# Optimization experiments

Measured on AMD Instinct MI355X. Metric: run time of the kernel, lower is better.

Reference implementation:

```python
import jax, jax.numpy as jnp
import numpy as np

N = 50000      # num_nodes
E = 300000     # edges per edge type
T = 3          # num_edge_type
C = 2          # num_channels
F_IN = 64      # feature_size
HID = 64       # hidden_size (w_out)
NL = 2         # num_layers (GT layers per FastGTN)
BETA = 0.5     # gtn_beta
TP = 0.8       # teleport_probability


def setup_inputs() -> dict:
    key = jax.random.key(0)
    ks = jax.random.split(key, 16)
    X = jax.random.normal(ks[0], (N, F_IN), dtype=jnp.float32)
    edge_index_0 = jax.random.randint(ks[1], (2, E), 0, N)
    edge_index_1 = jax.random.randint(ks[2], (2, E), 0, N)
    edge_index_2 = jax.random.randint(ks[3], (2, E), 0, N)
    edge_value_0 = jax.random.uniform(ks[4], (E,), dtype=jnp.float32)
    edge_value_1 = jax.random.uniform(ks[5], (E,), dtype=jnp.float32)
    edge_value_2 = jax.random.uniform(ks[6], (E,), dtype=jnp.float32)
    # glorot for Ws (per-channel projection), std=0.1 for GT layer mixing weights
    g0 = np.sqrt(6.0 / (F_IN + HID))
    g1 = np.sqrt(6.0 / (HID + HID))
    Ws0 = jax.random.uniform(ks[7], (C, F_IN, HID), minval=-g0, maxval=g0, dtype=jnp.float32)
    Ws1 = jax.random.uniform(ks[8], (C, HID, HID), minval=-g1, maxval=g1, dtype=jnp.float32)
    layerW0 = 0.1 * jax.random.normal(ks[9], (NL, C, T), dtype=jnp.float32)
    layerW1 = 0.1 * jax.random.normal(ks[10], (NL, C, T), dtype=jnp.float32)
    gl = np.sqrt(1.0 / (C * HID))
    lin_W0 = jax.random.uniform(ks[11], (C * HID, HID), minval=-gl, maxval=gl, dtype=jnp.float32)
    lin_b0 = jax.random.uniform(ks[12], (HID,), minval=-gl, maxval=gl, dtype=jnp.float32)
    lin_W1 = jax.random.uniform(ks[13], (C * HID, HID), minval=-gl, maxval=gl, dtype=jnp.float32)
    lin_b1 = jax.random.uniform(ks[14], (HID,), minval=-gl, maxval=gl, dtype=jnp.float32)
    return dict(X=X,
                edge_value_0=edge_value_0, edge_value_1=edge_value_1, edge_value_2=edge_value_2,
                Ws0=Ws0, Ws1=Ws1, layerW0=layerW0, layerW1=layerW1,
                lin_W0=lin_W0, lin_b0=lin_b0, lin_W1=lin_W1, lin_b1=lin_b1,
                edge_index_0=edge_index_0, edge_index_1=edge_index_1, edge_index_2=edge_index_2)


def _spmm_mix(H, filt, vals, etype, row, col):
    # H: [C, N, d]; filt: [C, T] softmaxed; vals: [Etot]; etype/row/col: [Etot]
    # == for each channel c: sum_j filt[c,j] * (A_j @ H[c])
    w = vals[None, :] * filt[:, etype]          # [C, Etot]
    msg = w[:, :, None] * H[:, col, :]          # [C, Etot, d]
    return jax.vmap(lambda m: jax.ops.segment_sum(m, row, num_segments=N))(msg)


def _fastgtn_block(Xin, Ws, layerW, linW, linb, row, col, vals, etype):
    H = jnp.einsum('nf,cfo->cno', Xin, Ws)      # [C, N, HID]
    X0 = jax.lax.stop_gradient(H)               # X_ = H.clone().detach()
    for l in range(NL):
        filt = jax.nn.softmax(layerW[l], axis=1)
        H = _spmm_mix(H, filt, vals, etype, row, col)
    Hm = TP * jax.nn.relu(BETA * X0 + (1.0 - BETA) * H) + (1.0 - TP) * X0
    Hm = jnp.transpose(Hm, (1, 0, 2)).reshape(N, C * Hm.shape[-1])  # [N, C*HID]
    return jax.nn.relu(Hm @ linW + linb)


def reference(X, edge_value_0, edge_value_1, edge_value_2,
              Ws0, Ws1, layerW0, layerW1,
              lin_W0, lin_b0, lin_W1, lin_b1,
              edge_index_0, edge_index_1, edge_index_2):
    row = jnp.concatenate([edge_index_0[0], edge_index_1[0], edge_index_2[0]])
    col = jnp.concatenate([edge_index_0[1], edge_index_1[1], edge_index_2[1]])
    vals = jnp.concatenate([edge_value_0, edge_value_1, edge_value_2])
    etype = jnp.repeat(jnp.arange(T), E)
    H = _fastgtn_block(X, Ws0, layerW0, lin_W0, lin_b0, row, col, vals, etype)
    H = _fastgtn_block(H, Ws1, layerW1, lin_W1, lin_b1, row, col, vals, etype)
    return H
```

## Files before the change

### kernel.cpp

```cpp
#include <hip/hip_runtime.h>
#include <hip/hip_fp16.h>

#define NN 50000
#define EE 300000
#define ETOT (3 * EE)
#define HD 64
#define RB 256
#define NB 196
#define CHUNK 8192
#define NBLKT ((EE + CHUNK - 1) / CHUNK)
#define NBT (3 * NBLKT)
#define NTOT (NB * NBT)
#define GS_VPT ((NTOT + 1023) / 1024)
#define MAXB 6144
#define PROJ_NTILE (NN / 16)
#define PP_GRID (NBT + 512)


__global__ void __launch_bounds__(256)
hist1_kernel(const int* __restrict__ ei0, const int* __restrict__ ei1,
             const int* __restrict__ ei2, int* __restrict__ hist) {
    __shared__ int lh[NB];
    int t = blockIdx.y;
    const int* ei = (t == 0) ? ei0 : (t == 1) ? ei1 : ei2;
    int tid = threadIdx.x;
    for (int i = tid; i < NB; i += 256) lh[i] = 0;
    __syncthreads();
    int e0 = blockIdx.x * CHUNK;
    for (int it = 0; it < CHUNK / 256; ++it) {
        int e = e0 + it * 256 + tid;
        if (e < EE) atomicAdd(&lh[ei[e] >> 8], 1);
    }
    __syncthreads();
    int flat = t * NBLKT + blockIdx.x;
    for (int i = tid; i < NB; i += 256) hist[i * NBT + flat] = lh[i];
}

__global__ void __launch_bounds__(1024)
gscan_kernel(const int* __restrict__ hist, int* __restrict__ gbase,
             int* __restrict__ bbase, int* __restrict__ rp,
             const float* __restrict__ lw0, const float* __restrict__ lw1,
             float* __restrict__ filt) {
    __shared__ int wsum[16];
    int tid = threadIdx.x, lane = tid & 63, wv = tid >> 6;
    if (tid < 8) {
        int b = tid >> 2, l = (tid >> 1) & 1, c = tid & 1;
        const float* lw = (b == 0 ? lw0 : lw1) + l * 6 + c * 3;
        float a0 = lw[0], a1 = lw[1], a2 = lw[2];
        float m  = fmaxf(a0, fmaxf(a1, a2));
        float e0 = expf(a0 - m), e1 = expf(a1 - m), e2 = expf(a2 - m);
        float s  = e0 + e1 + e2;
        float* o = filt + tid * 3;
        o[0] = e0 / s; o[1] = e1 / s; o[2] = e2 / s;
    }
    int s0 = tid * GS_VPT;
    int local = 0;
    for (int j = 0; j < GS_VPT; ++j) {
        int s = s0 + j;
        if (s < NTOT) local += hist[s];
    }
    int x = local;
#pragma unroll
    for (int d = 1; d < 64; d <<= 1) {
        int y = __shfl_up(x, d);
        if (lane >= d) x += y;
    }
    if (lane == 63) wsum[wv] = x;
    __syncthreads();
    if (tid == 0) {
        int s = 0;
        for (int i = 0; i < 16; ++i) { int t = wsum[i]; wsum[i] = s; s += t; }
    }
    __syncthreads();
    int run = x + wsum[wv] - local;
    for (int j = 0; j < GS_VPT; ++j) {
        int s = s0 + j;
        if (s < NTOT) {
            gbase[s] = run;
            int bucket = s / NBT;
            if (s - bucket * NBT == 0) bbase[bucket] = run;
            run += hist[s];
        }
    }
    if (tid == 0) { bbase[NB] = ETOT; rp[NN] = ETOT; }
}

__global__ void __launch_bounds__(256)
place_proj_kernel(const int* __restrict__ ei0, const int* __restrict__ ei1,
                  const int* __restrict__ ei2,
                  const float* __restrict__ ev0, const float* __restrict__ ev1,
                  const float* __restrict__ ev2,
                  const int* __restrict__ gbase, uint2* __restrict__ staged,
                  const float* __restrict__ Xin, const float* __restrict__ Ws,
                  __half2* __restrict__ Hh) {
    __shared__ float Wl[2 * 64 * 64];
    __shared__ float Xs[16 * 65];
    __shared__ int   lbase[NB];
    int tid = threadIdx.x;

    if (blockIdx.x < NBT) {
        int flat = blockIdx.x;
        int t  = flat / NBLKT;
        int bx = flat - t * NBLKT;
        const int*   ei = (t == 0) ? ei0 : (t == 1) ? ei1 : ei2;
        const float* ev = (t == 0) ? ev0 : (t == 1) ? ev1 : ev2;
        for (int i = tid; i < NB; i += 256) lbase[i] = gbase[i * NBT + flat];
        __syncthreads();
        int e0 = bx * CHUNK;
        for (int it = 0; it < CHUNK / 256; ++it) {
            int e = e0 + it * 256 + tid;
            if (e < EE) {
                int row = ei[e];
                int col = ei[EE + e];
                unsigned int q = (unsigned int)__float2int_rn(ev[e] * 16383.0f);
                unsigned int mw = (unsigned int)col | ((unsigned int)t << 16) | (q << 18);
                int pos = atomicAdd(&lbase[row >> 8], 1);
                staged[pos] = make_uint2(mw, (unsigned int)row);
            }
        }
    } else {
        for (int i = tid; i < 2 * 64 * 64; i += 256) Wl[i] = Ws[i];
        int oq = (tid & 15) * 4;
        int ln = tid >> 4;
        for (int tile = blockIdx.x - NBT; tile < PROJ_NTILE; tile += 512) {
            int n0 = tile * 16;
            __syncthreads();
            for (int i = tid; i < 16 * 64; i += 256)
                Xs[(i >> 6) * 65 + (i & 63)] = Xin[(n0 + (i >> 6)) * 64 + (i & 63)];
            __syncthreads();
            float a0[4] = {0.f, 0.f, 0.f, 0.f};
            float a1[4] = {0.f, 0.f, 0.f, 0.f};
            for (int f = 0; f < 64; ++f) {
                float  x  = Xs[ln * 65 + f];
                float4 w0 = *(const float4*)&Wl[f * 64 + oq];
                float4 w1 = *(const float4*)&Wl[4096 + f * 64 + oq];
                a0[0] += x * w0.x; a0[1] += x * w0.y;
                a0[2] += x * w0.z; a0[3] += x * w0.w;
                a1[0] += x * w1.x; a1[1] += x * w1.y;
                a1[2] += x * w1.z; a1[3] += x * w1.w;
            }
            float4 o4;
            ((__half2*)&o4)[0] = __floats2half2_rn(a0[0], a1[0]);
            ((__half2*)&o4)[1] = __floats2half2_rn(a0[1], a1[1]);
            ((__half2*)&o4)[2] = __floats2half2_rn(a0[2], a1[2]);
            ((__half2*)&o4)[3] = __floats2half2_rn(a0[3], a1[3]);
            *(float4*)&Hh[(n0 + ln) * HD + oq] = o4;
        }
    }
}

__global__ void __launch_bounds__(256)
csr_kernel(const uint2* __restrict__ staged, const int* __restrict__ bbase,
           int* __restrict__ rp, unsigned int* __restrict__ meta) {
    __shared__ int hist[RB];
    __shared__ int lcur[RB];
    __shared__ int wsum[4];
    __shared__ unsigned int metaL[MAXB];
    int b   = blockIdx.x;
    int tid = threadIdx.x;
    int base = bbase[b];
    int cnt  = bbase[b + 1] - base;
    int row0 = b * RB;

    hist[tid] = 0;
    __syncthreads();
    for (int i = tid; i < cnt; i += 256) {
        uint2 s = staged[base + i];
        atomicAdd(&hist[(int)s.y - row0], 1);
    }
    __syncthreads();
    int lane = tid & 63, wv = tid >> 6;
    int v = hist[tid];
    int x = v;
#pragma unroll
    for (int d = 1; d < 64; d <<= 1) {
        int y = __shfl_up(x, d);
        if (lane >= d) x += y;
    }
    if (lane == 63) wsum[wv] = x;
    __syncthreads();
    if (tid == 0) {
        int s = 0;
        for (int i = 0; i < 4; ++i) { int t = wsum[i]; wsum[i] = s; s += t; }
    }
    __syncthreads();
    int excl = x + wsum[wv] - v;
    lcur[tid] = excl;
    int row = row0 + tid;
    if (row < NN) rp[row] = base + excl;
    __syncthreads();
    for (int i = tid; i < cnt; i += 256) {
        uint2 s = staged[base + i];
        int p = atomicAdd(&lcur[(int)s.y - row0], 1);
        metaL[p] = s.x;
    }
    __syncthreads();
    for (int i = tid; i < cnt; i += 256)
        meta[base + i] = metaL[i];
}

__device__ __forceinline__ void edge_acc(unsigned int mm, float4 r,
                                         float F00, float F01, float F02,
                                         float F10, float F11, float F12,
                                         float* accA, float* accB) {
    int   et = (mm >> 16) & 3;
    float q  = (float)(mm >> 18);
    float w0 = q * ((et == 0) ? F00 : (et == 1) ? F01 : F02);
    float w1 = q * ((et == 0) ? F10 : (et == 1) ? F11 : F12);
#pragma unroll
    for (int i = 0; i < 4; ++i) {
        float2 x = __half22float2(((const __half2*)&r)[i]);
        accA[i] += w0 * x.x;
        accB[i] += w1 * x.y;
    }
}

__global__ void __launch_bounds__(256)
spmm_kernel(const float4* __restrict__ Hin4, float4* __restrict__ Hout4,
            const unsigned int* __restrict__ meta, const int* __restrict__ rp,
            const float* __restrict__ filt ) {
    const int wid  = threadIdx.x >> 6;
    const int lane = threadIdx.x & 63;
    const int g    = lane >> 4;
    const int fq   = lane & 15;
    const int row  = blockIdx.x * 4 + wid;

    const float s = 1.0f / 16383.0f;
    const float F00 = filt[0] * s, F01 = filt[1] * s, F02 = filt[2] * s;
    const float F10 = filt[3] * s, F11 = filt[4] * s, F12 = filt[5] * s;

    float accA[4] = {0.f, 0.f, 0.f, 0.f};
    float accB[4] = {0.f, 0.f, 0.f, 0.f};

    const int beg = rp[row], end = rp[row + 1];
    for (int j0 = beg; j0 < end; j0 += 64) {
        int cnt = min(end - j0, 64);
        unsigned int m = (lane < cnt) ? meta[j0 + lane] : 0u;
        for (int k = 0; k < cnt; k += 24) {
            unsigned int mmA = (unsigned int)__shfl((int)m, k + g);
            unsigned int mmB = (unsigned int)__shfl((int)m, k + 4 + g);
            float4 rA = Hin4[(mmA & 0xffffu) * 16 + fq];
            float4 rB = Hin4[(mmB & 0xffffu) * 16 + fq];
            if (k + 16 < cnt) {
                unsigned int mmC = (unsigned int)__shfl((int)m, k + 8 + g);
                unsigned int mmD = (unsigned int)__shfl((int)m, k + 12 + g);
                unsigned int mmE = (unsigned int)__shfl((int)m, k + 16 + g);
                unsigned int mmF = (unsigned int)__shfl((int)m, k + 20 + g);
                float4 rC = Hin4[(mmC & 0xffffu) * 16 + fq];
                float4 rD = Hin4[(mmD & 0xffffu) * 16 + fq];
                float4 rE = Hin4[(mmE & 0xffffu) * 16 + fq];
                float4 rF = Hin4[(mmF & 0xffffu) * 16 + fq];
                edge_acc(mmA, rA, F00, F01, F02, F10, F11, F12, accA, accB);
                edge_acc(mmB, rB, F00, F01, F02, F10, F11, F12, accA, accB);
                edge_acc(mmC, rC, F00, F01, F02, F10, F11, F12, accA, accB);
                edge_acc(mmD, rD, F00, F01, F02, F10, F11, F12, accA, accB);
                edge_acc(mmE, rE, F00, F01, F02, F10, F11, F12, accA, accB);
                edge_acc(mmF, rF, F00, F01, F02, F10, F11, F12, accA, accB);
            } else if (k + 8 < cnt) {
                unsigned int mmC = (unsigned int)__shfl((int)m, k + 8 + g);
                unsigned int mmD = (unsigned int)__shfl((int)m, k + 12 + g);
                float4 rC = Hin4[(mmC & 0xffffu) * 16 + fq];
                float4 rD = Hin4[(mmD & 0xffffu) * 16 + fq];
                edge_acc(mmA, rA, F00, F01, F02, F10, F11, F12, accA, accB);
                edge_acc(mmB, rB, F00, F01, F02, F10, F11, F12, accA, accB);
                edge_acc(mmC, rC, F00, F01, F02, F10, F11, F12, accA, accB);
                edge_acc(mmD, rD, F00, F01, F02, F10, F11, F12, accA, accB);
            } else {
                edge_acc(mmA, rA, F00, F01, F02, F10, F11, F12, accA, accB);
                edge_acc(mmB, rB, F00, F01, F02, F10, F11, F12, accA, accB);
            }
        }
    }
#pragma unroll
    for (int i = 0; i < 4; ++i) {
        accA[i] += __shfl_xor(accA[i], 16); accA[i] += __shfl_xor(accA[i], 32);
        accB[i] += __shfl_xor(accB[i], 16); accB[i] += __shfl_xor(accB[i], 32);
    }
    if (g == 0) {
        float4 o4;
        ((__half2*)&o4)[0] = __floats2half2_rn(accA[0], accB[0]);
        ((__half2*)&o4)[1] = __floats2half2_rn(accA[1], accB[1]);
        ((__half2*)&o4)[2] = __floats2half2_rn(accA[2], accB[2]);
        ((__half2*)&o4)[3] = __floats2half2_rn(accA[3], accB[3]);
        Hout4[row * 16 + fq] = o4;
    }
}

#define EPI_TILE 64
#define HS_STRIDE 133
template<bool PROJ>
__global__ void __launch_bounds__(256, 4)
epilogue_kernel(const __half2* __restrict__ X0, const __half2* __restrict__ H,
                const float* __restrict__ linW, const float* __restrict__ linb,
                const float* __restrict__ Wsn, float* __restrict__ out,
                __half2* __restrict__ X0out) {
    __shared__ float Hs[EPI_TILE * HS_STRIDE];
    int tid = threadIdx.x;
    int oc = (tid & 15) * 4;
    int nq = tid >> 4;
    float bias[4];
#pragma unroll
    for (int i = 0; i < 4; ++i) bias[i] = linb[oc + i];
    const int ntiles = (NN + EPI_TILE - 1) / EPI_TILE;
    for (int tile = blockIdx.x; tile < ntiles; tile += gridDim.x) {
        int n0 = tile * EPI_TILE;
        __syncthreads();
        for (int i = tid; i < EPI_TILE * 64; i += 256) {
            int ln = i >> 6, d = i & 63;
            int n = n0 + ln;
            float2 x0 = make_float2(0.f, 0.f), h = make_float2(0.f, 0.f);
            if (n < NN) {
                x0 = __half22float2(X0[n * HD + d]);
                h  = __half22float2(H [n * HD + d]);
            }
            float z0 = fmaxf(0.5f * x0.x + 0.5f * h.x, 0.f);
            float z1 = fmaxf(0.5f * x0.y + 0.5f * h.y, 0.f);
            Hs[ln * HS_STRIDE + d]      = 0.8f * z0 + 0.2f * x0.x;
            Hs[ln * HS_STRIDE + 64 + d] = 0.8f * z1 + 0.2f * x0.y;
        }
        __syncthreads();
        float acc[4][4];
#pragma unroll
        for (int j = 0; j < 4; ++j)
#pragma unroll
            for (int i = 0; i < 4; ++i) acc[j][i] = bias[i];
        for (int k = 0; k < 128; ++k) {
            float4 w4 = *(const float4*)&linW[k * 64 + oc];
#pragma unroll
            for (int j = 0; j < 4; ++j) {
                float x = Hs[(nq + 16 * j) * HS_STRIDE + k];
                acc[j][0] += x * w4.x; acc[j][1] += x * w4.y;
                acc[j][2] += x * w4.z; acc[j][3] += x * w4.w;
            }
        }
        if (!PROJ) {
#pragma unroll
            for (int j = 0; j < 4; ++j) {
                int n = n0 + nq + 16 * j;
                if (n < NN) {
#pragma unroll
                    for (int i = 0; i < 4; ++i)
                        out[n * HD + oc + i] = fmaxf(acc[j][i], 0.f);
                }
            }
        } else {
            __syncthreads();
#pragma unroll
            for (int j = 0; j < 4; ++j)
#pragma unroll
                for (int i = 0; i < 4; ++i)
                    Hs[(nq + 16 * j) * HS_STRIDE + oc + i] =
                        fmaxf(acc[j][i], 0.f);
            __syncthreads();
            float p0[4][4], p1[4][4];
#pragma unroll
            for (int j = 0; j < 4; ++j)
#pragma unroll
                for (int i = 0; i < 4; ++i) { p0[j][i] = 0.f; p1[j][i] = 0.f; }
            for (int f = 0; f < 64; ++f) {
                float4 w0 = *(const float4*)&Wsn[f * 64 + oc];
                float4 w1 = *(const float4*)&Wsn[4096 + f * 64 + oc];
#pragma unroll
                for (int j = 0; j < 4; ++j) {
                    float x = Hs[(nq + 16 * j) * HS_STRIDE + f];
                    p0[j][0] += x * w0.x; p0[j][1] += x * w0.y;
                    p0[j][2] += x * w0.z; p0[j][3] += x * w0.w;
                    p1[j][0] += x * w1.x; p1[j][1] += x * w1.y;
                    p1[j][2] += x * w1.z; p1[j][3] += x * w1.w;
                }
            }
#pragma unroll
            for (int j = 0; j < 4; ++j) {
                int n = n0 + nq + 16 * j;
                if (n < NN) {
                    float4 o4;
                    ((__half2*)&o4)[0] = __floats2half2_rn(p0[j][0], p1[j][0]);
                    ((__half2*)&o4)[1] = __floats2half2_rn(p0[j][1], p1[j][1]);
                    ((__half2*)&o4)[2] = __floats2half2_rn(p0[j][2], p1[j][2]);
                    ((__half2*)&o4)[3] = __floats2half2_rn(p0[j][3], p1[j][3]);
                    *(float4*)&X0out[n * HD + oc] = o4;
                }
            }
        }
    }
}

extern "C" void kernel_launch(void* const* d_in, const int* in_sizes, int n_in,
                              void* d_out, int out_size, void* d_ws, size_t ws_size,
                              hipStream_t stream) {
    const float* X     = (const float*)d_in[0];
    const float* ev0   = (const float*)d_in[1];
    const float* ev1   = (const float*)d_in[2];
    const float* ev2   = (const float*)d_in[3];
    const float* Ws0   = (const float*)d_in[4];
    const float* Ws1   = (const float*)d_in[5];
    const float* lw0   = (const float*)d_in[6];
    const float* lw1   = (const float*)d_in[7];
    const float* linW0 = (const float*)d_in[8];
    const float* linb0 = (const float*)d_in[9];
    const float* linW1 = (const float*)d_in[10];
    const float* linb1 = (const float*)d_in[11];
    const int*   ei0   = (const int*)d_in[12];
    const int*   ei1   = (const int*)d_in[13];
    const int*   ei2   = (const int*)d_in[14];
    float* out = (float*)d_out;

    float* ws = (float*)d_ws;
    __half2* X0h = (__half2*)(ws);
    __half2* Ha  = (__half2*)(ws + 1 * NN * HD);
    __half2* Hb  = (__half2*)(ws + 2 * NN * HD);
    uint2*   staged = (uint2*)(ws + 3 * NN * HD);
    float*   filt   = ws + 4 * NN * HD;
    int*     hist   = (int*)(filt + 32);
    int*     gbase  = hist + NTOT;
    int*     bbase  = gbase + NTOT;
    int*     rp     = bbase + NB + 4;
    unsigned int* meta = (unsigned int*)(rp + NN + 16);

    dim3 egrid(NBLKT, 3);
    hist1_kernel<<<egrid, 256, 0, stream>>>(ei0, ei1, ei2, hist);
    gscan_kernel<<<1, 1024, 0, stream>>>(hist, gbase, bbase, rp,
                                         lw0, lw1, filt);
    place_proj_kernel<<<PP_GRID, 256, 0, stream>>>(ei0, ei1, ei2,
                                                   ev0, ev1, ev2,
                                                   gbase, staged,
                                                   X, Ws0, X0h);
    csr_kernel<<<NB, 256, 0, stream>>>(staged, bbase, rp, meta);

    spmm_kernel<<<NN / 4, 256, 0, stream>>>((const float4*)X0h, (float4*)Ha,
                                            meta, rp, filt + 0);
    spmm_kernel<<<NN / 4, 256, 0, stream>>>((const float4*)Ha, (float4*)Hb,
                                            meta, rp, filt + 6);
    epilogue_kernel<true><<<784, 256, 0, stream>>>(X0h, Hb, linW0, linb0,
                                                   Ws1, nullptr, X0h);

    spmm_kernel<<<NN / 4, 256, 0, stream>>>((const float4*)X0h, (float4*)Ha,
                                            meta, rp, filt + 12);
    spmm_kernel<<<NN / 4, 256, 0, stream>>>((const float4*)Ha, (float4*)Hb,
                                            meta, rp, filt + 18);
    epilogue_kernel<false><<<784, 256, 0, stream>>>(X0h, Hb, linW1, linb1,
                                                    Ws1, out, nullptr);
}
```

Measured before the change: 356.0 us.

## Move input projection from place kernel into CSR build kernel

Splits the combined edge-placement/projection kernel into a standalone place kernel and merges the projection blocks into the CSR-build kernel instead. The projection now co-runs with the per-bucket CSR sort rather than with edge placement. It also stops staging the Ws weights in shared memory and reads them straight from global memory, cutting shared memory use so more blocks can be resident alongside the large metaL buffer. The risk is more global/cache traffic for weight reads and uneven load, since only 196 CSR blocks share the launch with 512 projection blocks.

```diff
diff --git a/kernel.cpp b/kernel.cpp
--- a/kernel.cpp
+++ b/kernel.cpp
@@ -14,7 +14,7 @@
 #define GS_VPT ((NTOT + 1023) / 1024)
 #define MAXB 6144
 #define PROJ_NTILE (NN / 16)
-#define PP_GRID (NBT + 512)
+#define CP_GRID (NB + 512)
 
 
 __global__ void __launch_bounds__(256)
@@ -86,43 +86,91 @@
 }
 
 __global__ void __launch_bounds__(256)
-place_proj_kernel(const int* __restrict__ ei0, const int* __restrict__ ei1,
-                  const int* __restrict__ ei2,
-                  const float* __restrict__ ev0, const float* __restrict__ ev1,
-                  const float* __restrict__ ev2,
-                  const int* __restrict__ gbase, uint2* __restrict__ staged,
-                  const float* __restrict__ Xin, const float* __restrict__ Ws,
-                  __half2* __restrict__ Hh) {
-    __shared__ float Wl[2 * 64 * 64];
+place_kernel(const int* __restrict__ ei0, const int* __restrict__ ei1,
+             const int* __restrict__ ei2,
+             const float* __restrict__ ev0, const float* __restrict__ ev1,
+             const float* __restrict__ ev2,
+             const int* __restrict__ gbase, uint2* __restrict__ staged) {
+    __shared__ int lbase[NB];
+    int tid = threadIdx.x;
+    int flat = blockIdx.x;
+    int t  = flat / NBLKT;
+    int bx = flat - t * NBLKT;
+    const int*   ei = (t == 0) ? ei0 : (t == 1) ? ei1 : ei2;
+    const float* ev = (t == 0) ? ev0 : (t == 1) ? ev1 : ev2;
+    for (int i = tid; i < NB; i += 256) lbase[i] = gbase[i * NBT + flat];
+    __syncthreads();
+    int e0 = bx * CHUNK;
+    for (int it = 0; it < CHUNK / 256; ++it) {
+        int e = e0 + it * 256 + tid;
+        if (e < EE) {
+            int row = ei[e];
+            int col = ei[EE + e];
+            unsigned int q = (unsigned int)__float2int_rn(ev[e] * 16383.0f);
+            unsigned int mw = (unsigned int)col | ((unsigned int)t << 16) | (q << 18);
+            int pos = atomicAdd(&lbase[row >> 8], 1);
+            staged[pos] = make_uint2(mw, (unsigned int)row);
+        }
+    }
+}
+
+__global__ void __launch_bounds__(256)
+csrproj_kernel(const uint2* __restrict__ staged, const int* __restrict__ bbase,
+               int* __restrict__ rp, unsigned int* __restrict__ meta,
+               const float* __restrict__ Xin, const float* __restrict__ Ws,
+               __half2* __restrict__ Hh) {
+    __shared__ int histL[RB];
+    __shared__ int lcur[RB];
+    __shared__ int wsum[4];
+    __shared__ unsigned int metaL[MAXB];
     __shared__ float Xs[16 * 65];
-    __shared__ int   lbase[NB];
     int tid = threadIdx.x;
 
-    if (blockIdx.x < NBT) {
-        int flat = blockIdx.x;
-        int t  = flat / NBLKT;
-        int bx = flat - t * NBLKT;
-        const int*   ei = (t == 0) ? ei0 : (t == 1) ? ei1 : ei2;
-        const float* ev = (t == 0) ? ev0 : (t == 1) ? ev1 : ev2;
-        for (int i = tid; i < NB; i += 256) lbase[i] = gbase[i * NBT + flat];
-        __syncthreads();
-        int e0 = bx * CHUNK;
-        for (int it = 0; it < CHUNK / 256; ++it) {
-            int e = e0 + it * 256 + tid;
-            if (e < EE) {
-                int row = ei[e];
-                int col = ei[EE + e];
-                unsigned int q = (unsigned int)__float2int_rn(ev[e] * 16383.0f);
-                unsigned int mw = (unsigned int)col | ((unsigned int)t << 16) | (q << 18);
-                int pos = atomicAdd(&lbase[row >> 8], 1);
-                staged[pos] = make_uint2(mw, (unsigned int)row);
-            }
-        }
+    if (blockIdx.x < NB) {
+        int b   = blockIdx.x;
+        int base = bbase[b];
+        int cnt  = bbase[b + 1] - base;
+        int row0 = b * RB;
+
+        histL[tid] = 0;
+        __syncthreads();
+        for (int i = tid; i < cnt; i += 256) {
+            uint2 s = staged[base + i];
+            atomicAdd(&histL[(int)s.y - row0], 1);
+        }
+        __syncthreads();
+        int lane = tid & 63, wv = tid >> 6;
+        int v = histL[tid];
+        int x = v;
+#pragma unroll
+        for (int d = 1; d < 64; d <<= 1) {
+            int y = __shfl_up(x, d);
+            if (lane >= d) x += y;
+        }
+        if (lane == 63) wsum[wv] = x;
+        __syncthreads();
+        if (tid == 0) {
+            int s = 0;
+            for (int i = 0; i < 4; ++i) { int t = wsum[i]; wsum[i] = s; s += t; }
+        }
+        __syncthreads();
+        int excl = x + wsum[wv] - v;
+        lcur[tid] = excl;
+        int row = row0 + tid;
+        if (row < NN) rp[row] = base + excl;
+        __syncthreads();
+        for (int i = tid; i < cnt; i += 256) {
+            uint2 s = staged[base + i];
+            int p = atomicAdd(&lcur[(int)s.y - row0], 1);
+            metaL[p] = s.x;
+        }
+        __syncthreads();
+        for (int i = tid; i < cnt; i += 256)
+            meta[base + i] = metaL[i];
     } else {
-        for (int i = tid; i < 2 * 64 * 64; i += 256) Wl[i] = Ws[i];
         int oq = (tid & 15) * 4;
         int ln = tid >> 4;
-        for (int tile = blockIdx.x - NBT; tile < PROJ_NTILE; tile += 512) {
+        for (int tile = blockIdx.x - NB; tile < PROJ_NTILE; tile += 512) {
             int n0 = tile * 16;
             __syncthreads();
             for (int i = tid; i < 16 * 64; i += 256)
@@ -132,8 +180,8 @@
             float a1[4] = {0.f, 0.f, 0.f, 0.f};
             for (int f = 0; f < 64; ++f) {
                 float  x  = Xs[ln * 65 + f];
-                float4 w0 = *(const float4*)&Wl[f * 64 + oq];
-                float4 w1 = *(const float4*)&Wl[4096 + f * 64 + oq];
+                float4 w0 = *(const float4*)&Ws[f * 64 + oq];
+                float4 w1 = *(const float4*)&Ws[4096 + f * 64 + oq];
                 a0[0] += x * w0.x; a0[1] += x * w0.y;
                 a0[2] += x * w0.z; a0[3] += x * w0.w;
                 a1[0] += x * w1.x; a1[1] += x * w1.y;
@@ -147,56 +195,6 @@
             *(float4*)&Hh[(n0 + ln) * HD + oq] = o4;
         }
     }
-}
-
-__global__ void __launch_bounds__(256)
-csr_kernel(const uint2* __restrict__ staged, const int* __restrict__ bbase,
-           int* __restrict__ rp, unsigned int* __restrict__ meta) {
-    __shared__ int hist[RB];
-    __shared__ int lcur[RB];
-    __shared__ int wsum[4];
-    __shared__ unsigned int metaL[MAXB];
-    int b   = blockIdx.x;
-    int tid = threadIdx.x;
-    int base = bbase[b];
-    int cnt  = bbase[b + 1] - base;
-    int row0 = b * RB;
-
-    hist[tid] = 0;
-    __syncthreads();
-    for (int i = tid; i < cnt; i += 256) {
-        uint2 s = staged[base + i];
-        atomicAdd(&hist[(int)s.y - row0], 1);
-    }
-    __syncthreads();
-    int lane = tid & 63, wv = tid >> 6;
-    int v = hist[tid];
-    int x = v;
-#pragma unroll
-    for (int d = 1; d < 64; d <<= 1) {
-        int y = __shfl_up(x, d);
-        if (lane >= d) x += y;
-    }
-    if (lane == 63) wsum[wv] = x;
-    __syncthreads();
-    if (tid == 0) {
-        int s = 0;
-        for (int i = 0; i < 4; ++i) { int t = wsum[i]; wsum[i] = s; s += t; }
-    }
-    __syncthreads();
-    int excl = x + wsum[wv] - v;
-    lcur[tid] = excl;
-    int row = row0 + tid;
-    if (row < NN) rp[row] = base + excl;
-    __syncthreads();
-    for (int i = tid; i < cnt; i += 256) {
-        uint2 s = staged[base + i];
-        int p = atomicAdd(&lcur[(int)s.y - row0], 1);
-        metaL[p] = s.x;
-    }
-    __syncthreads();
-    for (int i = tid; i < cnt; i += 256)
-        meta[base + i] = metaL[i];
 }
 
 __device__ __forceinline__ void edge_acc(unsigned int mm, float4 r,
@@ -421,11 +419,10 @@
     hist1_kernel<<<egrid, 256, 0, stream>>>(ei0, ei1, ei2, hist);
     gscan_kernel<<<1, 1024, 0, stream>>>(hist, gbase, bbase, rp,
                                          lw0, lw1, filt);
-    place_proj_kernel<<<PP_GRID, 256, 0, stream>>>(ei0, ei1, ei2,
-                                                   ev0, ev1, ev2,
-                                                   gbase, staged,
-                                                   X, Ws0, X0h);
-    csr_kernel<<<NB, 256, 0, stream>>>(staged, bbase, rp, meta);
+    place_kernel<<<NBT, 256, 0, stream>>>(ei0, ei1, ei2, ev0, ev1, ev2,
+                                          gbase, staged);
+    csrproj_kernel<<<CP_GRID, 256, 0, stream>>>(staged, bbase, rp, meta,
+                                                X, Ws0, X0h);
 
     spmm_kernel<<<NN / 4, 256, 0, stream>>>((const float4*)X0h, (float4*)Ha,
                                             meta, rp, filt + 0);
```

Result: slower. 391.9 us (+10.1%).
